# Kernel tuning notes

Hardware: AMD Instinct MI355X
Metric: run time of the kernel (lower is better)

Reference implementation:

```python
import jax, jax.numpy as jnp
import numpy as np

N_VERTICES = 500_000
N_EDGES = 16_000_000


def setup_inputs() -> dict:
    key = jax.random.key(0)
    k1, k2, k3 = jax.random.split(key, 3)
    # positive features keep A_ii and the scatter-sum denominator away from zero
    vertex_attr = jax.random.uniform(k1, (N_VERTICES, 2), dtype=jnp.float32, minval=0.1, maxval=1.1)
    edge_attr = jax.random.uniform(k2, (N_EDGES, 3), dtype=jnp.float32, minval=0.1, maxval=1.1)
    edgeij_pair = jax.random.randint(k3, (2, N_EDGES), 0, N_VERTICES, dtype=jnp.int32)
    return {"vertex_attr": vertex_attr, "edge_attr": edge_attr, "edgeij_pair": edgeij_pair}


def reference(vertex_attr, edge_attr, edgeij_pair):
    src = edgeij_pair[0]  # i (row) in PyG MetaLayer convention
    n_vertices = vertex_attr.shape[0]

    A_ij = edge_attr[:, 0]
    S_ij = edge_attr[:, 1]
    v_ij = edge_attr[:, 2]
    # (Layer1_EdgeUpdate appends w_ij = C_j as a 4th edge column, but that
    #  column is never read downstream, so it is omitted here.)

    # Layer1 vertex update: gammabar_i = sum_k A_ik / sum_k A_ik*S_ik*v_ik
    numerator = jax.ops.segment_sum(A_ij, src, num_segments=n_vertices)
    denominator = jax.ops.segment_sum(A_ij * S_ij * v_ij, src, num_segments=n_vertices)
    gammabar = numerator / denominator  # [N]

    A_ii = vertex_attr[:, 0]
    C_i = vertex_attr[:, 1]
    alpha = gammabar / A_ii  # [N]

    # Layer2 edge update: w_ij = (1 - C_i) * (-A_ij * alpha_i), i = src
    w_ij = (1.0 - C_i[src]) * (-A_ij * alpha[src])  # [E]
    return w_ij
```

## Files before the change

kernel.cpp:

```cpp
#include <hip/hip_runtime.h>


#define BINS 256
#define VSHIFT 11
#define VPB 2048
#define NBLK 1024
#define BT 256
#define SBT 512
#define SUB 2048
#define SPLIT 8
#define CAP 16

#define SC_A 524288.0f
#define SC_D 4194304.0f

typedef unsigned int u32;
typedef unsigned short u16;
typedef unsigned long long u64;

static __device__ __forceinline__ u32 f2h(float x) {
    _Float16 h = (_Float16)x; u16 u; __builtin_memcpy(&u, &h, 2); return (u32)u;
}
static __device__ __forceinline__ float h2f(u32 u) {
    u16 v = (u16)u; _Float16 h; __builtin_memcpy(&h, &v, 2); return (float)h;
}


__global__ void hist_k(const int* __restrict__ src, int ne, int chunk,
                       u32* __restrict__ bh) {
    __shared__ u32 h[BINS];
    for (int j = threadIdx.x; j < BINS; j += SBT) h[j] = 0;
    __syncthreads();
    int lo = blockIdx.x * chunk;
    int hi = min(ne, lo + chunk);
    int n = hi - lo;
    int ngroups = (n + 3) >> 2;
    for (int g = threadIdx.x; g < ngroups; g += SBT) {
        int i = lo + (g << 2);
        if (i + 3 < hi) {
            int4 s = *reinterpret_cast<const int4*>(src + i);
            atomicAdd(&h[((u32)s.x) >> VSHIFT], 1u);
            atomicAdd(&h[((u32)s.y) >> VSHIFT], 1u);
            atomicAdd(&h[((u32)s.z) >> VSHIFT], 1u);
            atomicAdd(&h[((u32)s.w) >> VSHIFT], 1u);
        } else {
            for (int j = i; j < hi; ++j)
                atomicAdd(&h[((u32)src[j]) >> VSHIFT], 1u);
        }
    }
    __syncthreads();
    for (int j = threadIdx.x; j < BINS; j += SBT)
        bh[(size_t)blockIdx.x * BINS + j] = h[j];
}

__global__ void scan_col_k(u32* __restrict__ bh, u32* __restrict__ bin_total) {
    const int IT = NBLK / BT;
    int bin = blockIdx.x, t = threadIdx.x;
    u32 v[IT];
    u32 tsum = 0;
    #pragma unroll
    for (int k = 0; k < IT; ++k) {
        v[k] = bh[(size_t)(IT * t + k) * BINS + bin];
        tsum += v[k];
    }
    int lane = t & 63, wv = t >> 6;
    u32 inc = tsum;
    #pragma unroll
    for (int d = 1; d < 64; d <<= 1) {
        u32 y = __shfl_up(inc, d);
        if (lane >= d) inc += y;
    }
    __shared__ u32 wsum[BT / 64];
    if (lane == 63) wsum[wv] = inc;
    __syncthreads();
    u32 wbase = 0;
    for (int w = 0; w < wv; ++w) wbase += wsum[w];
    u32 run = wbase + inc - tsum;
    #pragma unroll
    for (int k = 0; k < IT; ++k) {
        u32 c = v[k];
        bh[(size_t)(IT * t + k) * BINS + bin] = run;
        run += c;
    }
    if (t == BT - 1) bin_total[bin] = run;
}

__global__ void scan_bins_k(const u32* __restrict__ bin_total,
                            u32* __restrict__ bin_base) {
    int t = threadIdx.x;
    u32 a0 = (t < BINS) ? bin_total[t] : 0;
    int lane = t & 63, wv = t >> 6;
    u32 inc = a0;
    #pragma unroll
    for (int d = 1; d < 64; d <<= 1) {
        u32 y = __shfl_up(inc, d);
        if (lane >= d) inc += y;
    }
    __shared__ u32 wsum[BT / 64];
    if (lane == 63) wsum[wv] = inc;
    __syncthreads();
    u32 wbase = 0;
    for (int w = 0; w < wv; ++w) wbase += wsum[w];
    if (t < BINS) bin_base[t] = wbase + inc - a0;
    if (t == BINS - 1) bin_base[BINS] = wbase + inc;
}

__global__ __launch_bounds__(SBT, 2)
void scatter_k(const float* __restrict__ eattr,
               const int* __restrict__ src,
               const u32* __restrict__ bh,
               const u32* __restrict__ bin_base,
               uint2* __restrict__ rec,
               u16* __restrict__ ah,
               int ne, int chunk) {
    __shared__ u32 cur[BINS];
    __shared__ u32 cnt[BINS];
    __shared__ uint2 stage[BINS * CAP];
    int t = threadIdx.x;
    int lo = blockIdx.x * chunk;
    int hi = min(ne, lo + chunk);
    if (lo >= hi) return;
    for (int j = t; j < BINS; j += SBT)
        cur[j] = bin_base[j] + bh[(size_t)blockIdx.x * BINS + j];

    float erA[12], erB[12];
    int srA[4], srB[4];

    auto LOADV = [&](int base, float* er, int* sr) {
        int o = t << 2;
        int n = min(hi - base, SUB);
        int i = base + o;
        if (o + 3 < n) {
            int4 s4 = *reinterpret_cast<const int4*>(src + i);
            sr[0] = s4.x; sr[1] = s4.y; sr[2] = s4.z; sr[3] = s4.w;
            const float4* ea = reinterpret_cast<const float4*>(eattr + 3ll * i);
            float4 w0 = ea[0], w1 = ea[1], w2 = ea[2];
            er[0] = w0.x; er[1] = w0.y; er[2]  = w0.z; er[3]  = w0.w;
            er[4] = w1.x; er[5] = w1.y; er[6]  = w1.z; er[7]  = w1.w;
            er[8] = w2.x; er[9] = w2.y; er[10] = w2.z; er[11] = w2.w;
        } else {
            #pragma unroll
            for (int j = 0; j < 4; ++j) {
                if (o + j < n) {
                    sr[j] = src[i + j];
                    er[3 * j]     = eattr[3ll * (i + j)];
                    er[3 * j + 1] = eattr[3ll * (i + j) + 1];
                    er[3 * j + 2] = eattr[3ll * (i + j) + 2];
                }
            }
        }
    };

    auto PLACE = [&](int base, float* er, int* sr) {
        int o = t << 2;
        int n = min(hi - base, SUB);
        ushort4 hv;
        u16* hp = &hv.x;
        #pragma unroll
        for (int j = 0; j < 4; ++j) {
            if (o + j < n) {
                u32 s = (u32)sr[j];
                float a = er[3 * j];
                float d = a * er[3 * j + 1] * er[3 * j + 2];
                u32 ni = __float2uint_rn(a * SC_A);
                u32 di = __float2uint_rn(d * SC_D);
                u32 b = s >> VSHIFT;
                uint2 pay = make_uint2(di, (ni << VSHIFT) | (s & (VPB - 1)));
                hp[j] = (u16)f2h(a);
                u32 slot = atomicAdd(&cnt[b], 1u);
                if (slot < CAP) stage[(b << 4) | slot] = pay;
                else rec[cur[b] + slot] = pay;
            }
        }
        if (o + 3 < n) {
            *reinterpret_cast<ushort4*>(ah + base + o) = hv;
        } else {
            #pragma unroll
            for (int j = 0; j < 4; ++j)
                if (o + j < n) ah[base + o + j] = hp[j];
        }
    };

    LOADV(lo, erA, srA);
    for (int base = lo; base < hi; base += SUB) {
        if (t < BINS) cnt[t] = 0;
        __syncthreads();
        PLACE(base, erA, srA);
        if (base + SUB < hi) LOADV(base + SUB, erB, srB);
        __syncthreads();
        #pragma unroll
        for (int r = 0; r < (BINS * CAP) / SBT; ++r) {
            int j = t + r * SBT;
            u32 b = (u32)j >> 4, s = (u32)j & 15u;
            u32 c = cnt[b];
            if (s < min(c, (u32)CAP)) rec[cur[b] + s] = stage[j];
        }
        __syncthreads();
        if (t < BINS) cur[t] += cnt[t];
        #pragma unroll
        for (int j = 0; j < 12; ++j) erA[j] = erB[j];
        #pragma unroll
        for (int j = 0; j < 4; ++j) srA[j] = srB[j];
    }
}

__global__ void accum_part_k(const uint2* __restrict__ rec,
                             const u32* __restrict__ bin_base,
                             u64* __restrict__ partial) {
    __shared__ u64 acc[VPB];
    int bin = blockIdx.x / SPLIT;
    int q   = blockIdx.x % SPLIT;
    for (int l = threadIdx.x; l < VPB; l += BT) acc[l] = 0ull;
    __syncthreads();
    u32 s0 = bin_base[bin], s1 = bin_base[bin + 1];
    u32 cnt = s1 - s0;
    u32 ra = s0 + (u32)((u64)cnt * q / SPLIT);
    u32 rb = s0 + (u32)((u64)cnt * (q + 1) / SPLIT);
    for (u32 r = ra + threadIdx.x; r < rb; r += BT) {
        uint2 qq = rec[r];
        u64 add = ((u64)(qq.y >> VSHIFT) << 35) | (u64)qq.x;
        atomicAdd(&acc[qq.y & (VPB - 1)], add);
    }
    __syncthreads();
    u64* po = partial + (size_t)blockIdx.x * VPB;
    for (int l = threadIdx.x; l < VPB; l += BT) po[l] = acc[l];
}

__global__ void coef_part_k(const u64* __restrict__ partial,
                            const float* __restrict__ vattr,
                            float* __restrict__ coef, int nv) {
    int v = blockIdx.x * blockDim.x + threadIdx.x;
    int stride = gridDim.x * blockDim.x;
    for (; v < nv; v += stride) {
        int bin = v >> VSHIFT, l = v & (VPB - 1);
        size_t base = ((size_t)bin * SPLIT << VSHIFT) + l;
        float num = 0.f, den = 0.f;
        #pragma unroll
        for (int sp = 0; sp < SPLIT; ++sp) {
            u64 p = partial[base + ((size_t)sp << VSHIFT)];
            num += (float)(u32)(p >> 32);
            den += (float)(u32)p;
        }
        float2 va = reinterpret_cast<const float2*>(vattr)[v];
        float gam = num / den;
        coef[v] = (1.0f - va.y) * (-gam / va.x);
    }
}


#define FPSCALE 8388608.0f
#define FPINV   (1.0f / 8388608.0f)

__global__ void zero_u64(u64* __restrict__ p, int n) {
    int i = blockIdx.x * blockDim.x + threadIdx.x;
    int stride = gridDim.x * blockDim.x;
    for (; i < n; i += stride) p[i] = 0ull;
}

__global__ void accum_packed(const float* __restrict__ eattr,
                             const int* __restrict__ src,
                             u64* __restrict__ accp,
                             u16* __restrict__ ah, int ne) {
    int t = blockIdx.x * blockDim.x + threadIdx.x;
    int stride = gridDim.x * blockDim.x;
    for (int i = t; i < ne; i += stride) {
        float a = eattr[3ll * i];
        float d = a * eattr[3ll * i + 1] * eattr[3ll * i + 2];
        u32 ni = (u32)__float2uint_rn(a * FPSCALE);
        u32 di = (u32)__float2uint_rn(d * FPSCALE);
        atomicAdd(&accp[(u32)src[i]], ((u64)ni << 32) | (u64)di);
        if (ah) ah[i] = (u16)f2h(a);
    }
}

__global__ void coef_packed(const float* __restrict__ vattr,
                            const u64* __restrict__ accp,
                            float* __restrict__ coef, int nv) {
    int v = blockIdx.x * blockDim.x + threadIdx.x;
    int stride = gridDim.x * blockDim.x;
    for (; v < nv; v += stride) {
        u64 a = accp[v];
        float num = (float)(u32)(a >> 32) * FPINV;
        float den = (float)(u32)a * FPINV;
        float2 va = reinterpret_cast<const float2*>(vattr)[v];
        coef[v] = (1.0f - va.y) * (-(num / den) / va.x);
    }
}


__global__ void finalize(const u16* __restrict__ ah,
                         const float* __restrict__ edge_attr,
                         const int* __restrict__ src,
                         const float* __restrict__ coef,
                         float* __restrict__ out, int ne4, int n_edges) {
    int t = blockIdx.x * blockDim.x + threadIdx.x;
    int stride = gridDim.x * blockDim.x;
    for (int i = t; i < ne4; i += stride) {
        int4 s = reinterpret_cast<const int4*>(src)[i];
        float4 A;
        if (ah) {
            ushort4 h = reinterpret_cast<const ushort4*>(ah)[i];
            A.x = h2f(h.x); A.y = h2f(h.y); A.z = h2f(h.z); A.w = h2f(h.w);
        } else {
            const float* e = edge_attr + 12ll * i;
            A.x = e[0]; A.y = e[3]; A.z = e[6]; A.w = e[9];
        }
        float4 w;
        w.x = coef[s.x] * A.x;
        w.y = coef[s.y] * A.y;
        w.z = coef[s.z] * A.z;
        w.w = coef[s.w] * A.w;
        reinterpret_cast<float4*>(out)[i] = w;
    }
    for (int e = 4 * ne4 + t; e < n_edges; e += stride) {
        float Ae = ah ? h2f(ah[e]) : edge_attr[3ll * e];
        out[e] = coef[src[e]] * Ae;
    }
}

extern "C" void kernel_launch(void* const* d_in, const int* in_sizes, int n_in,
                              void* d_out, int out_size, void* d_ws, size_t ws_size,
                              hipStream_t stream) {
    const float* vattr = (const float*)d_in[0];
    const float* eattr = (const float*)d_in[1];
    const int*   pair  = (const int*)d_in[2];
    int nv = in_sizes[0] / 2;
    int ne = in_sizes[1] / 3;
    const int* src = pair;
    float* out = (float*)d_out;

    int ne4 = ne / 4;
    auto capped = [](long long want, int cap) {
        return (int)(want < cap ? (want > 1 ? want : 1) : cap);
    };
    int fgrid = capped(((long long)ne4 + BT - 1) / BT, 4096);

    size_t off = 0;
    float* coef = (float*)((char*)d_ws + off); off += (size_t)nv * 4;
    off = (off + 255) & ~(size_t)255;
    u32* bin_total = (u32*)((char*)d_ws + off); off += (size_t)BINS * 4;
    u32* bin_base  = (u32*)((char*)d_ws + off); off += (size_t)(BINS + 1) * 4;
    off = (off + 255) & ~(size_t)255;
    u32* bh  = (u32*)((char*)d_ws + off); off += (size_t)NBLK * BINS * 4;
    off = (off + 255) & ~(size_t)255;
    u64* partial = (u64*)((char*)d_ws + off); off += ((size_t)BINS * SPLIT << VSHIFT) * 8;
    off = (off + 255) & ~(size_t)255;
    uint2* rec = (uint2*)((char*)d_ws + off); off += 8ull * ne;
    off = (off + 255) & ~(size_t)255;
    u16* ah = (u16*)((char*)d_ws + off); off += 2ull * ne;
    long long chunk_ll = ((((long long)ne + NBLK - 1) / NBLK) + SUB - 1) / SUB * SUB;
    bool main_ok = ws_size >= off && nv <= (BINS << VSHIFT) &&
                   chunk_ll * NBLK < 2147000000ll;
    int chunk = (int)chunk_ll;

    if (main_ok) {
        hist_k<<<NBLK, SBT, 0, stream>>>(src, ne, chunk, bh);
        scan_col_k<<<BINS, BT, 0, stream>>>(bh, bin_total);
        scan_bins_k<<<1, BT, 0, stream>>>(bin_total, bin_base);
        scatter_k<<<NBLK, SBT, 0, stream>>>(eattr, src, bh, bin_base, rec, ah, ne, chunk);
        accum_part_k<<<BINS * SPLIT, BT, 0, stream>>>(rec, bin_base, partial);
        coef_part_k<<<capped(((long long)nv + BT - 1) / BT, 2048), BT, 0, stream>>>(partial, vattr, coef, nv);
        finalize<<<fgrid, BT, 0, stream>>>(ah, eattr, src, coef, out, ne4, ne);
    } else {
        u64* accp = (u64*)d_ws;
        float* fcoef = (float*)(accp + nv);
        size_t fb_base = (size_t)nv * 12;
        fb_base = (fb_base + 255) & ~(size_t)255;
        u16* fah = nullptr;
        if (ws_size >= fb_base + 2ull * ne)
            fah = (u16*)((char*)d_ws + fb_base);
        int zgrid = capped(((long long)nv + BT - 1) / BT, 2048);
        int agrid = capped(((long long)ne + BT - 1) / BT, 4096);
        int cgrid = capped(((long long)nv + BT - 1) / BT, 2048);
        zero_u64<<<zgrid, BT, 0, stream>>>(accp, nv);
        accum_packed<<<agrid, BT, 0, stream>>>(eattr, src, accp, fah, ne);
        coef_packed<<<cgrid, BT, 0, stream>>>(vattr, accp, fcoef, nv);
        finalize<<<fgrid, BT, 0, stream>>>(fah, eattr, src, fcoef, out, ne4, ne);
    }
}
```

Before: 280.3 us.

## Replace global histogram and scans with per-bin atomic slot reservation

Drops the separate histogram and two scan kernels. Each scatter block now counts its own bins in shared memory and reserves 16-aligned ranges in fixed-capacity per-bin regions through global atomics, then pads the unused tail of each range with zero records. Accumulation reads each bin region up to its atomic cursor. This removes two kernel launches and a pass over src plus the bh traffic, at the cost of a larger workspace, padding writes, and a capacity guard on per-bin counts.

```diff
diff --git a/kernel.cpp b/kernel.cpp
--- a/kernel.cpp
+++ b/kernel.cpp
@@ -10,6 +10,7 @@
 #define SUB 2048
 #define SPLIT 8
 #define CAP 16
+#define C_PER_BIN 76800u
 
 #define SC_A 524288.0f
 #define SC_D 4194304.0f
@@ -26,102 +27,53 @@
 }
 
 
-__global__ void hist_k(const int* __restrict__ src, int ne, int chunk,
-                       u32* __restrict__ bh) {
-    __shared__ u32 h[BINS];
-    for (int j = threadIdx.x; j < BINS; j += SBT) h[j] = 0;
-    __syncthreads();
-    int lo = blockIdx.x * chunk;
-    int hi = min(ne, lo + chunk);
-    int n = hi - lo;
-    int ngroups = (n + 3) >> 2;
-    for (int g = threadIdx.x; g < ngroups; g += SBT) {
-        int i = lo + (g << 2);
-        if (i + 3 < hi) {
-            int4 s = *reinterpret_cast<const int4*>(src + i);
-            atomicAdd(&h[((u32)s.x) >> VSHIFT], 1u);
-            atomicAdd(&h[((u32)s.y) >> VSHIFT], 1u);
-            atomicAdd(&h[((u32)s.z) >> VSHIFT], 1u);
-            atomicAdd(&h[((u32)s.w) >> VSHIFT], 1u);
-        } else {
-            for (int j = i; j < hi; ++j)
-                atomicAdd(&h[((u32)src[j]) >> VSHIFT], 1u);
-        }
-    }
-    __syncthreads();
-    for (int j = threadIdx.x; j < BINS; j += SBT)
-        bh[(size_t)blockIdx.x * BINS + j] = h[j];
-}
-
-__global__ void scan_col_k(u32* __restrict__ bh, u32* __restrict__ bin_total) {
-    const int IT = NBLK / BT;
-    int bin = blockIdx.x, t = threadIdx.x;
-    u32 v[IT];
-    u32 tsum = 0;
-    #pragma unroll
-    for (int k = 0; k < IT; ++k) {
-        v[k] = bh[(size_t)(IT * t + k) * BINS + bin];
-        tsum += v[k];
-    }
-    int lane = t & 63, wv = t >> 6;
-    u32 inc = tsum;
-    #pragma unroll
-    for (int d = 1; d < 64; d <<= 1) {
-        u32 y = __shfl_up(inc, d);
-        if (lane >= d) inc += y;
-    }
-    __shared__ u32 wsum[BT / 64];
-    if (lane == 63) wsum[wv] = inc;
-    __syncthreads();
-    u32 wbase = 0;
-    for (int w = 0; w < wv; ++w) wbase += wsum[w];
-    u32 run = wbase + inc - tsum;
-    #pragma unroll
-    for (int k = 0; k < IT; ++k) {
-        u32 c = v[k];
-        bh[(size_t)(IT * t + k) * BINS + bin] = run;
-        run += c;
-    }
-    if (t == BT - 1) bin_total[bin] = run;
-}
-
-__global__ void scan_bins_k(const u32* __restrict__ bin_total,
-                            u32* __restrict__ bin_base) {
-    int t = threadIdx.x;
-    u32 a0 = (t < BINS) ? bin_total[t] : 0;
-    int lane = t & 63, wv = t >> 6;
-    u32 inc = a0;
-    #pragma unroll
-    for (int d = 1; d < 64; d <<= 1) {
-        u32 y = __shfl_up(inc, d);
-        if (lane >= d) inc += y;
-    }
-    __shared__ u32 wsum[BT / 64];
-    if (lane == 63) wsum[wv] = inc;
-    __syncthreads();
-    u32 wbase = 0;
-    for (int w = 0; w < wv; ++w) wbase += wsum[w];
-    if (t < BINS) bin_base[t] = wbase + inc - a0;
-    if (t == BINS - 1) bin_base[BINS] = wbase + inc;
+__global__ void zero_gcur_k(u32* __restrict__ gcur) {
+    if (threadIdx.x < BINS) gcur[threadIdx.x] = 0u;
 }
 
 __global__ __launch_bounds__(SBT, 2)
 void scatter_k(const float* __restrict__ eattr,
                const int* __restrict__ src,
-               const u32* __restrict__ bh,
-               const u32* __restrict__ bin_base,
+               u32* __restrict__ gcur,
                uint2* __restrict__ rec,
                u16* __restrict__ ah,
                int ne, int chunk) {
     __shared__ u32 cur[BINS];
     __shared__ u32 cnt[BINS];
+    __shared__ u32 cnt_all[BINS];
+    __shared__ u32 sstart[BINS];
     __shared__ uint2 stage[BINS * CAP];
     int t = threadIdx.x;
     int lo = blockIdx.x * chunk;
     int hi = min(ne, lo + chunk);
     if (lo >= hi) return;
-    for (int j = t; j < BINS; j += SBT)
-        cur[j] = bin_base[j] + bh[(size_t)blockIdx.x * BINS + j];
+
+    if (t < BINS) cnt_all[t] = 0u;
+    __syncthreads();
+    {
+        int n = hi - lo;
+        int ng = (n + 3) >> 2;
+        for (int g = t; g < ng; g += SBT) {
+            int i = lo + (g << 2);
+            if (i + 3 < hi) {
+                int4 s = *reinterpret_cast<const int4*>(src + i);
+                atomicAdd(&cnt_all[((u32)s.x) >> VSHIFT], 1u);
+                atomicAdd(&cnt_all[((u32)s.y) >> VSHIFT], 1u);
+                atomicAdd(&cnt_all[((u32)s.z) >> VSHIFT], 1u);
+                atomicAdd(&cnt_all[((u32)s.w) >> VSHIFT], 1u);
+            } else {
+                for (int j = i; j < hi; ++j)
+                    atomicAdd(&cnt_all[((u32)src[j]) >> VSHIFT], 1u);
+            }
+        }
+    }
+    __syncthreads();
+    if (t < BINS) {
+        u32 p = (cnt_all[t] + 15u) & ~15u;
+        u32 s0 = p ? atomicAdd(&gcur[t], p) : 0u;
+        sstart[t] = s0;
+        cur[t] = s0;
+    }
 
     float erA[12], erB[12];
     int srA[4], srB[4];
@@ -169,7 +121,7 @@
                 hp[j] = (u16)f2h(a);
                 u32 slot = atomicAdd(&cnt[b], 1u);
                 if (slot < CAP) stage[(b << 4) | slot] = pay;
-                else rec[cur[b] + slot] = pay;
+                else rec[(size_t)b * C_PER_BIN + cur[b] + slot] = pay;
             }
         }
         if (o + 3 < n) {
@@ -183,7 +135,7 @@
 
     LOADV(lo, erA, srA);
     for (int base = lo; base < hi; base += SUB) {
-        if (t < BINS) cnt[t] = 0;
+        if (t < BINS) cnt[t] = 0u;
         __syncthreads();
         PLACE(base, erA, srA);
         if (base + SUB < hi) LOADV(base + SUB, erB, srB);
@@ -193,7 +145,8 @@
             int j = t + r * SBT;
             u32 b = (u32)j >> 4, s = (u32)j & 15u;
             u32 c = cnt[b];
-            if (s < min(c, (u32)CAP)) rec[cur[b] + s] = stage[j];
+            if (s < min(c, (u32)CAP))
+                rec[(size_t)b * C_PER_BIN + cur[b] + s] = stage[j];
         }
         __syncthreads();
         if (t < BINS) cur[t] += cnt[t];
@@ -202,22 +155,27 @@
         #pragma unroll
         for (int j = 0; j < 4; ++j) srA[j] = srB[j];
     }
+    if (t < BINS) {
+        u32 end = sstart[t] + ((cnt_all[t] + 15u) & ~15u);
+        for (u32 i = cur[t]; i < end; ++i)
+            rec[(size_t)t * C_PER_BIN + i] = make_uint2(0u, 0u);
+    }
 }
 
 __global__ void accum_part_k(const uint2* __restrict__ rec,
-                             const u32* __restrict__ bin_base,
+                             const u32* __restrict__ gcur,
                              u64* __restrict__ partial) {
     __shared__ u64 acc[VPB];
     int bin = blockIdx.x / SPLIT;
     int q   = blockIdx.x % SPLIT;
     for (int l = threadIdx.x; l < VPB; l += BT) acc[l] = 0ull;
     __syncthreads();
-    u32 s0 = bin_base[bin], s1 = bin_base[bin + 1];
-    u32 cnt = s1 - s0;
-    u32 ra = s0 + (u32)((u64)cnt * q / SPLIT);
-    u32 rb = s0 + (u32)((u64)cnt * (q + 1) / SPLIT);
-    for (u32 r = ra + threadIdx.x; r < rb; r += BT) {
-        uint2 qq = rec[r];
+    u32 T = gcur[bin];
+    const uint2* rb_ = rec + (size_t)bin * C_PER_BIN;
+    u32 ra  = (u32)((u64)T * q / SPLIT);
+    u32 rbn = (u32)((u64)T * (q + 1) / SPLIT);
+    for (u32 r = ra + threadIdx.x; r < rbn; r += BT) {
+        uint2 qq = rb_[r];
         u64 add = ((u64)(qq.y >> VSHIFT) << 35) | (u64)qq.x;
         atomicAdd(&acc[qq.y & (VPB - 1)], add);
     }
@@ -338,27 +296,23 @@
     size_t off = 0;
     float* coef = (float*)((char*)d_ws + off); off += (size_t)nv * 4;
     off = (off + 255) & ~(size_t)255;
-    u32* bin_total = (u32*)((char*)d_ws + off); off += (size_t)BINS * 4;
-    u32* bin_base  = (u32*)((char*)d_ws + off); off += (size_t)(BINS + 1) * 4;
-    off = (off + 255) & ~(size_t)255;
-    u32* bh  = (u32*)((char*)d_ws + off); off += (size_t)NBLK * BINS * 4;
+    u32* gcur = (u32*)((char*)d_ws + off); off += (size_t)BINS * 4;
     off = (off + 255) & ~(size_t)255;
     u64* partial = (u64*)((char*)d_ws + off); off += ((size_t)BINS * SPLIT << VSHIFT) * 8;
     off = (off + 255) & ~(size_t)255;
-    uint2* rec = (uint2*)((char*)d_ws + off); off += 8ull * ne;
+    uint2* rec = (uint2*)((char*)d_ws + off); off += (size_t)BINS * C_PER_BIN * 8;
     off = (off + 255) & ~(size_t)255;
     u16* ah = (u16*)((char*)d_ws + off); off += 2ull * ne;
     long long chunk_ll = ((((long long)ne + NBLK - 1) / NBLK) + SUB - 1) / SUB * SUB;
     bool main_ok = ws_size >= off && nv <= (BINS << VSHIFT) &&
-                   chunk_ll * NBLK < 2147000000ll;
+                   chunk_ll * NBLK < 2147000000ll &&
+                   (u32)(ne / BINS + NBLK * 8 + 4096) <= C_PER_BIN;
     int chunk = (int)chunk_ll;
 
     if (main_ok) {
-        hist_k<<<NBLK, SBT, 0, stream>>>(src, ne, chunk, bh);
-        scan_col_k<<<BINS, BT, 0, stream>>>(bh, bin_total);
-        scan_bins_k<<<1, BT, 0, stream>>>(bin_total, bin_base);
-        scatter_k<<<NBLK, SBT, 0, stream>>>(eattr, src, bh, bin_base, rec, ah, ne, chunk);
-        accum_part_k<<<BINS * SPLIT, BT, 0, stream>>>(rec, bin_base, partial);
+        zero_gcur_k<<<1, BINS, 0, stream>>>(gcur);
+        scatter_k<<<NBLK, SBT, 0, stream>>>(eattr, src, gcur, rec, ah, ne, chunk);
+        accum_part_k<<<BINS * SPLIT, BT, 0, stream>>>(rec, gcur, partial);
         coef_part_k<<<capped(((long long)nv + BT - 1) / BT, 2048), BT, 0, stream>>>(partial, vattr, coef, nv);
         finalize<<<fgrid, BT, 0, stream>>>(ah, eattr, src, coef, out, ne4, ne);
     } else {
```

Measured after the change: 310.5 us. +10.7%, slower.
